# Kernel tuning notes

Measured on AMD Instinct MI355X. Metric: run time of the kernel, lower is better.

The kernel has to match this reference:

```python
import jax, jax.numpy as jnp
import numpy as np

N, E = 50000, 800000
IN_DIM, HIDDEN, OUT_DIM, LAYERS = 128, 64, 40, 3


def setup_inputs() -> dict:
    key = jax.random.key(0)
    ks = jax.random.split(key, 12)
    glorot = lambda k, fi, fo: jax.random.normal(k, (fi, fo), jnp.float32) * np.sqrt(2.0 / (fi + fo)).astype(np.float32)
    return {
        "x": jax.random.normal(ks[0], (N, IN_DIM), jnp.float32),
        "edge_index": jax.random.randint(ks[1], (2, E), 0, N, jnp.int64),
        "edge_weight": jax.random.uniform(ks[2], (E,), jnp.float32),
        "W1": glorot(ks[3], IN_DIM, HIDDEN), "b1": jnp.zeros((HIDDEN,), jnp.float32),
        "W2": glorot(ks[4], HIDDEN, HIDDEN), "b2": jnp.zeros((HIDDEN,), jnp.float32),
        "W3": glorot(ks[5], HIDDEN, HIDDEN), "b3": jnp.zeros((HIDDEN,), jnp.float32),
        "Wlin": glorot(ks[6], HIDDEN * LAYERS, OUT_DIM), "blin": jnp.zeros((OUT_DIM,), jnp.float32),
    }


def reference(x, edge_index, edge_weight, W1, b1, W2, b2, W3, b3, Wlin, blin):
    src, dst = edge_index[0], edge_index[1]

    def gcn_conv(h, W, b):
        # GCNConv with normalize=False: linear transform, then weighted sum aggregation at dst, then bias.
        h = h @ W                                   # [N, hidden]
        msg = h[src] * edge_weight[:, None]          # [E, hidden] gather + scale
        agg = jax.ops.segment_sum(msg, dst, num_segments=h.shape[0])  # scatter-add
        return agg + b

    outs = []
    h = x
    for W, b in ((W1, b1), (W2, b2), (W3, b3)):
        h = jax.nn.relu(gcn_conv(h, W, b))           # dropout is identity at inference
        outs.append(h)

    hjk = jnp.concatenate(outs, axis=-1)             # JumpingKnowledge mode='cat' -> [N, hidden*layers]
    return hjk @ Wlin + blin                         # [N, out_dim]
```

## Files before the change

kernel.cpp:

```cpp
#include <hip/hip_runtime.h>

#define HID 64
#define JK_DIM 192
#define OUT_DIM 40
#define AP 136
#define HP 72

typedef __attribute__((ext_vector_type(8))) short bf16x8;
typedef __attribute__((ext_vector_type(4))) float f32x4;

__device__ inline unsigned short f2b(float f) {
    unsigned u = __float_as_uint(f);
    unsigned r = u + 0x7FFF + ((u >> 16) & 1);
    return (unsigned short)(r >> 16);
}
__device__ inline float b2f(unsigned short u) {
    return __uint_as_float(((unsigned)u) << 16);
}
__device__ inline float blo(unsigned u) { return __uint_as_float(u << 16); }
__device__ inline float bhi(unsigned u) { return __uint_as_float(u & 0xFFFF0000u); }
__device__ inline unsigned pack2(float a, float b) {
    return (unsigned)f2b(a) | ((unsigned)f2b(b) << 16);
}

__global__ __launch_bounds__(256) void hist_gemm(
        const int* __restrict__ dst, int* __restrict__ deg,
        unsigned short* __restrict__ rank, int E, int part,
        int nGemm, int histBlk,
        const float* __restrict__ x, const float* __restrict__ W1,
        unsigned short* __restrict__ linb, int n,
        const float* __restrict__ W2, const float* __restrict__ W3,
        const float* __restrict__ Wlin,
        unsigned short* __restrict__ W2T, unsigned short* __restrict__ W3T,
        unsigned short* __restrict__ WlinT) {
    __shared__ unsigned short Ah[64 * AP];
    __shared__ unsigned short Wt[64 * AP];
    int tid = threadIdx.x;
    int bid = blockIdx.x;
    if (bid >= nGemm + histBlk) {
        int base = (bid - nGemm - histBlk) * 256 + tid;
        int stride = 32 * 256;
        for (int i = base; i < 64 * 64; i += stride) {
            int nn = i >> 6, k = i & 63;
            W2T[i] = f2b(W2[k * 64 + nn]);
            W3T[i] = f2b(W3[k * 64 + nn]);
        }
        for (int i = base; i < 48 * JK_DIM; i += stride) {
            int c = i / JK_DIM, k = i - c * JK_DIM;
            WlinT[i] = (c < OUT_DIM) ? f2b(Wlin[k * OUT_DIM + c]) : (unsigned short)0;
        }
        return;
    }
    if (bid >= nGemm) {
        int hb = bid - nGemm;
        int p = hb & 7;
        int hbid = hb >> 3;
        int nblk = histBlk >> 3;
        int lo = p * part, hi = lo + part;
        int E4 = E >> 2;
        for (int q = hbid * 256 + tid; q < E4; q += nblk * 256) {
            int4 d4 = ((const int4*)dst)[q];
            int e = q * 4;
            if (d4.x >= lo && d4.x < hi) rank[e + 0] = (unsigned short)atomicAdd(&deg[d4.x], 1);
            if (d4.y >= lo && d4.y < hi) rank[e + 1] = (unsigned short)atomicAdd(&deg[d4.y], 1);
            if (d4.z >= lo && d4.z < hi) rank[e + 2] = (unsigned short)atomicAdd(&deg[d4.z], 1);
            if (d4.w >= lo && d4.w < hi) rank[e + 3] = (unsigned short)atomicAdd(&deg[d4.w], 1);
        }
        if (hbid == 0 && tid < (E & 3)) {
            int e = (E & ~3) + tid;
            int d = dst[e];
            if (d >= lo && d < hi) rank[e] = (unsigned short)atomicAdd(&deg[d], 1);
        }
        return;
    }
    int row0 = bid * 64;
    if (row0 >= n) return;
    for (int i = tid; i < 64 * 32; i += 256) {
        int r = i >> 5;
        int c4 = (i & 31) * 4;
        int grow = row0 + r;
        if (grow >= n) grow = n - 1;
        float4 v = *(const float4*)(x + (long)grow * 128 + c4);
        ushort4 o;
        o.x = f2b(v.x); o.y = f2b(v.y); o.z = f2b(v.z); o.w = f2b(v.w);
        *(ushort4*)(Ah + r * AP + c4) = o;
    }
    for (int i = tid; i < 128 * 16; i += 256) {
        int k = i >> 4;
        int n4 = (i & 15) * 4;
        float4 v = *(const float4*)(W1 + (long)k * 64 + n4);
        Wt[(n4 + 0) * AP + k] = f2b(v.x);
        Wt[(n4 + 1) * AP + k] = f2b(v.y);
        Wt[(n4 + 2) * AP + k] = f2b(v.z);
        Wt[(n4 + 3) * AP + k] = f2b(v.w);
    }
    __syncthreads();

    int wave = tid >> 6;
    int lane = tid & 63;
    int lr = lane & 15;
    int lk = (lane >> 4) * 8;
    f32x4 acc[4];
#pragma unroll
    for (int nf = 0; nf < 4; ++nf) acc[nf] = (f32x4){0.f, 0.f, 0.f, 0.f};
#pragma unroll
    for (int k0 = 0; k0 < 128; k0 += 32) {
        bf16x8 a = *(const bf16x8*)(Ah + (wave * 16 + lr) * AP + k0 + lk);
#pragma unroll
        for (int nf = 0; nf < 4; ++nf) {
            bf16x8 b = *(const bf16x8*)(Wt + (nf * 16 + lr) * AP + k0 + lk);
            acc[nf] = __builtin_amdgcn_mfma_f32_16x16x32_bf16(a, b, acc[nf], 0, 0, 0);
        }
    }
    int mbase = wave * 16 + (lane >> 4) * 4;
#pragma unroll
    for (int nf = 0; nf < 4; ++nf) {
#pragma unroll
        for (int r = 0; r < 4; ++r) {
            int grow = row0 + mbase + r;
            if (grow < n)
                linb[(long)grow * HID + nf * 16 + lr] = f2b(acc[nf][r]);
        }
    }
}

__global__ __launch_bounds__(256) void scan_fused(const int* __restrict__ deg,
                                                  int* __restrict__ off,
                                                  int* __restrict__ gctr, int n) {
    __shared__ int tmp[256];
    __shared__ int base;
    int i = blockIdx.x * 256 + threadIdx.x;
    int v = (i < n) ? deg[i] : 0;
    tmp[threadIdx.x] = v;
    __syncthreads();
    for (int d = 1; d < 256; d <<= 1) {
        int t = (threadIdx.x >= d) ? tmp[threadIdx.x - d] : 0;
        __syncthreads();
        tmp[threadIdx.x] += t;
        __syncthreads();
    }
    if (threadIdx.x == 255) base = atomicAdd(gctr, tmp[255]);
    __syncthreads();
    if (i < n) off[i] = base + tmp[threadIdx.x] - v;
}

__global__ __launch_bounds__(256) void fill_csr(
        const int* __restrict__ src, const int* __restrict__ dst,
        const float* __restrict__ ew, const int* __restrict__ off,
        const unsigned short* __restrict__ rank,
        unsigned* __restrict__ ecsr, int E) {
    int tid = threadIdx.x;
    int q = blockIdx.x * 256 + tid;
    int E4 = E >> 2;
    if (q < E4) {
        int4 d4 = ((const int4*)dst)[q];
        int4 s4 = ((const int4*)src)[q];
        float4 wv = ((const float4*)ew)[q];
        ushort4 r4 = ((const ushort4*)rank)[q];
        ecsr[off[d4.x] + r4.x] = (unsigned)s4.x | ((unsigned)f2b(wv.x) << 16);
        ecsr[off[d4.y] + r4.y] = (unsigned)s4.y | ((unsigned)f2b(wv.y) << 16);
        ecsr[off[d4.z] + r4.z] = (unsigned)s4.z | ((unsigned)f2b(wv.z) << 16);
        ecsr[off[d4.w] + r4.w] = (unsigned)s4.w | ((unsigned)f2b(wv.w) << 16);
    }
    if (blockIdx.x == 0 && tid < (E & 3)) {
        int e = (E & ~3) + tid;
        int d = dst[e];
        ecsr[off[d] + rank[e]] = (unsigned)src[e] | ((unsigned)f2b(ew[e]) << 16);
    }
}

__global__ __launch_bounds__(256) void aggregate(const unsigned short* __restrict__ linb,
                                                 const unsigned* __restrict__ ecsr,
                                                 const int* __restrict__ off,
                                                 const int* __restrict__ deg,
                                                 const float* __restrict__ bias,
                                                 unsigned short* __restrict__ hout, int n) {
    int cl = threadIdx.x & 7;
    float4 bLo = *(const float4*)(bias + cl * 8);
    float4 bHi = *(const float4*)(bias + cl * 8 + 4);
    int grp = (blockIdx.x * 256 + threadIdx.x) >> 3;
    int ngrp = (gridDim.x * 256) >> 3;
    for (int node = grp; node < n; node += ngrp) {
        int start = off[node];
        int cnt = deg[node];
        float acc[8];
#pragma unroll
        for (int i = 0; i < 8; ++i) acc[i] = 0.f;

        int s[8];
        float w[8];
#pragma unroll
        for (int t = 0; t < 8; ++t) {
            s[t] = 0; w[t] = 0.f;
            if (t < cnt) {
                unsigned m = ecsr[start + t];
                s[t] = (int)(m & 0xFFFFu);
                w[t] = b2f((unsigned short)(m >> 16));
            }
        }
        for (int bb = 0; bb < cnt; bb += 8) {
            int s2[8];
            float w2[8];
#pragma unroll
            for (int t = 0; t < 8; ++t) {
                int e = bb + 8 + t;
                s2[t] = 0; w2[t] = 0.f;
                if (e < cnt) {
                    unsigned m = ecsr[start + e];
                    s2[t] = (int)(m & 0xFFFFu);
                    w2[t] = b2f((unsigned short)(m >> 16));
                }
            }
            uint4 u[8];
#pragma unroll
            for (int t = 0; t < 8; ++t)
                u[t] = *(const uint4*)(linb + (long)s[t] * HID + cl * 8);
#pragma unroll
            for (int t = 0; t < 8; ++t) {
                acc[0] += blo(u[t].x) * w[t];
                acc[1] += bhi(u[t].x) * w[t];
                acc[2] += blo(u[t].y) * w[t];
                acc[3] += bhi(u[t].y) * w[t];
                acc[4] += blo(u[t].z) * w[t];
                acc[5] += bhi(u[t].z) * w[t];
                acc[6] += blo(u[t].w) * w[t];
                acc[7] += bhi(u[t].w) * w[t];
            }
#pragma unroll
            for (int t = 0; t < 8; ++t) { s[t] = s2[t]; w[t] = w2[t]; }
        }

        uint4 o;
        o.x = pack2(fmaxf(acc[0] + bLo.x, 0.f), fmaxf(acc[1] + bLo.y, 0.f));
        o.y = pack2(fmaxf(acc[2] + bLo.z, 0.f), fmaxf(acc[3] + bLo.w, 0.f));
        o.z = pack2(fmaxf(acc[4] + bHi.x, 0.f), fmaxf(acc[5] + bHi.y, 0.f));
        o.w = pack2(fmaxf(acc[6] + bHi.z, 0.f), fmaxf(acc[7] + bHi.w, 0.f));
        *(uint4*)(hout + (long)node * JK_DIM + cl * 8) = o;
    }
}

__global__ __launch_bounds__(256) void agg_transform(
        const unsigned short* __restrict__ hprev,
        const unsigned* __restrict__ ecsr,
        const int* __restrict__ off, const int* __restrict__ deg,
        const unsigned short* __restrict__ WT, const float* __restrict__ bias,
        unsigned short* __restrict__ hout, int n) {
    __shared__ unsigned short Hs[64 * HP];
    __shared__ unsigned short Wt[64 * HP];
    int tid = threadIdx.x;
    int row0 = blockIdx.x * 64;
    if (row0 >= n) return;
    for (int i = tid; i < 64 * 8; i += 256) {
        int nn = i >> 3;
        int k8 = (i & 7) * 8;
        *(uint4*)(Wt + nn * HP + k8) = *(const uint4*)(WT + nn * 64 + k8);
    }
    int cl = tid & 7;
    int g0 = tid >> 3;
    for (int gi = 0; gi < 2; ++gi) {
        int lrow = g0 + gi * 32;
        int node = row0 + lrow;
        float acc[8];
#pragma unroll
        for (int i = 0; i < 8; ++i) acc[i] = 0.f;
        if (node < n) {
            int start = off[node];
            int cnt = deg[node];
            int s[8];
            float w[8];
#pragma unroll
            for (int t = 0; t < 8; ++t) {
                s[t] = 0; w[t] = 0.f;
                if (t < cnt) {
                    unsigned m = ecsr[start + t];
                    s[t] = (int)(m & 0xFFFFu);
                    w[t] = b2f((unsigned short)(m >> 16));
                }
            }
            for (int bb = 0; bb < cnt; bb += 8) {
                int s2[8];
                float w2[8];
#pragma unroll
                for (int t = 0; t < 8; ++t) {
                    int e = bb + 8 + t;
                    s2[t] = 0; w2[t] = 0.f;
                    if (e < cnt) {
                        unsigned m = ecsr[start + e];
                        s2[t] = (int)(m & 0xFFFFu);
                        w2[t] = b2f((unsigned short)(m >> 16));
                    }
                }
                uint4 u[8];
#pragma unroll
                for (int t = 0; t < 8; ++t)
                    u[t] = *(const uint4*)(hprev + (long)s[t] * JK_DIM + cl * 8);
#pragma unroll
                for (int t = 0; t < 8; ++t) {
                    acc[0] += blo(u[t].x) * w[t];
                    acc[1] += bhi(u[t].x) * w[t];
                    acc[2] += blo(u[t].y) * w[t];
                    acc[3] += bhi(u[t].y) * w[t];
                    acc[4] += blo(u[t].z) * w[t];
                    acc[5] += bhi(u[t].z) * w[t];
                    acc[6] += blo(u[t].w) * w[t];
                    acc[7] += bhi(u[t].w) * w[t];
                }
#pragma unroll
                for (int t = 0; t < 8; ++t) { s[t] = s2[t]; w[t] = w2[t]; }
            }
        }
        uint4 o;
        o.x = pack2(acc[0], acc[1]);
        o.y = pack2(acc[2], acc[3]);
        o.z = pack2(acc[4], acc[5]);
        o.w = pack2(acc[6], acc[7]);
        *(uint4*)(Hs + lrow * HP + cl * 8) = o;
    }
    __syncthreads();
    int wave = tid >> 6;
    int lane = tid & 63;
    int lr = lane & 15;
    int lk = (lane >> 4) * 8;
    f32x4 d[4];
#pragma unroll
    for (int nf = 0; nf < 4; ++nf) d[nf] = (f32x4){0.f, 0.f, 0.f, 0.f};
#pragma unroll
    for (int k0 = 0; k0 < 64; k0 += 32) {
        bf16x8 a = *(const bf16x8*)(Hs + (wave * 16 + lr) * HP + k0 + lk);
#pragma unroll
        for (int nf = 0; nf < 4; ++nf) {
            bf16x8 b = *(const bf16x8*)(Wt + (nf * 16 + lr) * HP + k0 + lk);
            d[nf] = __builtin_amdgcn_mfma_f32_16x16x32_bf16(a, b, d[nf], 0, 0, 0);
        }
    }
    int mbase = wave * 16 + (lane >> 4) * 4;
#pragma unroll
    for (int nf = 0; nf < 4; ++nf) {
        float bv = bias[nf * 16 + lr];
#pragma unroll
        for (int r = 0; r < 4; ++r) {
            int grow = row0 + mbase + r;
            if (grow < n)
                hout[(long)grow * JK_DIM + nf * 16 + lr] = f2b(fmaxf(d[nf][r] + bv, 0.f));
        }
    }
}

__global__ __launch_bounds__(256) void jk_final(
        const unsigned short* __restrict__ hprev,
        const unsigned* __restrict__ ecsr,
        const int* __restrict__ off, const int* __restrict__ deg,
        const unsigned short* __restrict__ W3T, const float* __restrict__ bias,
        const unsigned short* __restrict__ hcat,
        const unsigned short* __restrict__ WlinT,
        const float* __restrict__ blin,
        float* __restrict__ outp, int n) {
    __shared__ unsigned short pool[128 * HP];
    unsigned short* Hs = pool;
    unsigned short* Wt = pool + 64 * HP;
    int tid = threadIdx.x;
    int row0 = blockIdx.x * 64;
    if (row0 >= n) return;
    for (int i = tid; i < 64 * 8; i += 256) {
        int nn = i >> 3;
        int k8 = (i & 7) * 8;
        *(uint4*)(Wt + nn * HP + k8) = *(const uint4*)(W3T + nn * 64 + k8);
    }
    int cl = tid & 7;
    int g0 = tid >> 3;
    for (int gi = 0; gi < 2; ++gi) {
        int lrow = g0 + gi * 32;
        int node = row0 + lrow;
        float acc[8];
#pragma unroll
        for (int i = 0; i < 8; ++i) acc[i] = 0.f;
        if (node < n) {
            int start = off[node];
            int cnt = deg[node];
            int s[8];
            float w[8];
#pragma unroll
            for (int t = 0; t < 8; ++t) {
                s[t] = 0; w[t] = 0.f;
                if (t < cnt) {
                    unsigned m = ecsr[start + t];
                    s[t] = (int)(m & 0xFFFFu);
                    w[t] = b2f((unsigned short)(m >> 16));
                }
            }
            for (int bb = 0; bb < cnt; bb += 8) {
                int s2[8];
                float w2[8];
#pragma unroll
                for (int t = 0; t < 8; ++t) {
                    int e = bb + 8 + t;
                    s2[t] = 0; w2[t] = 0.f;
                    if (e < cnt) {
                        unsigned m = ecsr[start + e];
                        s2[t] = (int)(m & 0xFFFFu);
                        w2[t] = b2f((unsigned short)(m >> 16));
                    }
                }
                uint4 u[8];
#pragma unroll
                for (int t = 0; t < 8; ++t)
                    u[t] = *(const uint4*)(hprev + (long)s[t] * JK_DIM + cl * 8);
#pragma unroll
                for (int t = 0; t < 8; ++t) {
                    acc[0] += blo(u[t].x) * w[t];
                    acc[1] += bhi(u[t].x) * w[t];
                    acc[2] += blo(u[t].y) * w[t];
                    acc[3] += bhi(u[t].y) * w[t];
                    acc[4] += blo(u[t].z) * w[t];
                    acc[5] += bhi(u[t].z) * w[t];
                    acc[6] += blo(u[t].w) * w[t];
                    acc[7] += bhi(u[t].w) * w[t];
                }
#pragma unroll
                for (int t = 0; t < 8; ++t) { s[t] = s2[t]; w[t] = w2[t]; }
            }
        }
        uint4 o;
        o.x = pack2(acc[0], acc[1]);
        o.y = pack2(acc[2], acc[3]);
        o.z = pack2(acc[4], acc[5]);
        o.w = pack2(acc[6], acc[7]);
        *(uint4*)(Hs + lrow * HP + cl * 8) = o;
    }
    __syncthreads();
    int wave = tid >> 6;
    int lane = tid & 63;
    int lr = lane & 15;
    int lk = (lane >> 4) * 8;
    f32x4 d[4];
#pragma unroll
    for (int nf = 0; nf < 4; ++nf) d[nf] = (f32x4){0.f, 0.f, 0.f, 0.f};
#pragma unroll
    for (int k0 = 0; k0 < 64; k0 += 32) {
        bf16x8 a = *(const bf16x8*)(Hs + (wave * 16 + lr) * HP + k0 + lk);
#pragma unroll
        for (int nf = 0; nf < 4; ++nf) {
            bf16x8 b = *(const bf16x8*)(Wt + (nf * 16 + lr) * HP + k0 + lk);
            d[nf] = __builtin_amdgcn_mfma_f32_16x16x32_bf16(a, b, d[nf], 0, 0, 0);
        }
    }
    int mbase = wave * 16 + (lane >> 4) * 4;
    unsigned short* As = Hs;
    unsigned short* WL = Wt;
    f32x4 acc2[3];
#pragma unroll
    for (int nf = 0; nf < 3; ++nf) acc2[nf] = (f32x4){0.f, 0.f, 0.f, 0.f};
    for (int ch = 0; ch < 2; ++ch) {
        int cb = ch * 64;
        __syncthreads();
        for (int i = tid; i < 64 * 8; i += 256) {
            int r = i >> 3;
            int q8 = (i & 7) * 8;
            int grow = row0 + r;
            if (grow >= n) grow = n - 1;
            *(uint4*)(As + r * HP + q8) = *(const uint4*)(hcat + (long)grow * JK_DIM + cb + q8);
        }
        for (int i = tid; i < 48 * 8; i += 256) {
            int c = i >> 3;
            int k8 = (i & 7) * 8;
            *(uint4*)(WL + c * HP + k8) = *(const uint4*)(WlinT + c * JK_DIM + cb + k8);
        }
        __syncthreads();
#pragma unroll
        for (int k0 = 0; k0 < 64; k0 += 32) {
            bf16x8 a = *(const bf16x8*)(As + (wave * 16 + lr) * HP + k0 + lk);
#pragma unroll
            for (int nf = 0; nf < 3; ++nf) {
                bf16x8 b = *(const bf16x8*)(WL + (nf * 16 + lr) * HP + k0 + lk);
                acc2[nf] = __builtin_amdgcn_mfma_f32_16x16x32_bf16(a, b, acc2[nf], 0, 0, 0);
            }
        }
    }
    __syncthreads();
#pragma unroll
    for (int nf = 0; nf < 4; ++nf) {
        float bv = bias[nf * 16 + lr];
#pragma unroll
        for (int r = 0; r < 4; ++r)
            As[(mbase + r) * HP + nf * 16 + lr] = f2b(fmaxf(d[nf][r] + bv, 0.f));
    }
    for (int i = tid; i < 48 * 8; i += 256) {
        int c = i >> 3;
        int k8 = (i & 7) * 8;
        *(uint4*)(WL + c * HP + k8) = *(const uint4*)(WlinT + c * JK_DIM + 128 + k8);
    }
    __syncthreads();
#pragma unroll
    for (int k0 = 0; k0 < 64; k0 += 32) {
        bf16x8 a = *(const bf16x8*)(As + (wave * 16 + lr) * HP + k0 + lk);
#pragma unroll
        for (int nf = 0; nf < 3; ++nf) {
            bf16x8 b = *(const bf16x8*)(WL + (nf * 16 + lr) * HP + k0 + lk);
            acc2[nf] = __builtin_amdgcn_mfma_f32_16x16x32_bf16(a, b, acc2[nf], 0, 0, 0);
        }
    }
#pragma unroll
    for (int nf = 0; nf < 3; ++nf) {
        int col = nf * 16 + lr;
        if (col < OUT_DIM) {
            float bb = blin[col];
#pragma unroll
            for (int r = 0; r < 4; ++r) {
                int grow = row0 + mbase + r;
                if (grow < n)
                    outp[(long)grow * OUT_DIM + col] = acc2[nf][r] + bb;
            }
        }
    }
}

extern "C" void kernel_launch(void* const* d_in, const int* in_sizes, int n_in,
                              void* d_out, int out_size, void* d_ws, size_t ws_size,
                              hipStream_t stream) {
    const float* x    = (const float*)d_in[0];
    const int*   ei   = (const int*)d_in[1];
    const float* ew   = (const float*)d_in[2];
    const float* W1   = (const float*)d_in[3];
    const float* b1   = (const float*)d_in[4];
    const float* W2   = (const float*)d_in[5];
    const float* b2   = (const float*)d_in[6];
    const float* W3   = (const float*)d_in[7];
    const float* b3   = (const float*)d_in[8];
    const float* Wlin = (const float*)d_in[9];
    const float* blin = (const float*)d_in[10];
    float* out = (float*)d_out;

    const int N = in_sizes[0] / 128;
    const int E = in_sizes[2];
    const int* src = ei;
    const int* dst = ei + E;
    const int PART = (N + 7) / 8;

    char* wsb = (char*)d_ws;
    unsigned short* linb  = (unsigned short*)wsb;   wsb += (long)N * HID * 2;
    unsigned short* hcatb = (unsigned short*)wsb;   wsb += (long)N * JK_DIM * 2;
    char* zbase = wsb;
    int* deg    = (int*)wsb;                        wsb += (long)N * 4;
    int* off    = (int*)wsb;                        wsb += (long)N * 4;
    int* bsum   = (int*)wsb;                        wsb += 256 * 4;
    size_t zbytes = (size_t)(wsb - zbase);
    unsigned short* W2T  = (unsigned short*)wsb;    wsb += 64 * 64 * 2;
    unsigned short* W3T  = (unsigned short*)wsb;    wsb += 64 * 64 * 2;
    unsigned short* WlinT = (unsigned short*)wsb;   wsb += 48 * JK_DIM * 2;
    unsigned* ecsr = (unsigned*)wsb;
    unsigned short* rank = hcatb;
    int* gctr = bsum;

    dim3 blk(256);
    const int nblkN = (N + 255) / 256;
    dim3 gN(nblkN);
    const int nGemm = (N + 63) / 64;
    const int histBlk = 8 * 104;
    dim3 gHG(nGemm + histBlk + 32);
    const int nFill = ((E >> 2) + 255) / 256;
    dim3 gFill(nFill);
    dim3 gTile((N + 63) / 64);
    dim3 gAgg((N + 31) / 32);

    unsigned short* h1 = hcatb;
    unsigned short* h2 = hcatb + HID;

    hipMemsetAsync(zbase, 0, zbytes, stream);

    hist_gemm<<<gHG, blk, 0, stream>>>(dst, deg, rank, E, PART, nGemm, histBlk,
                                       x, W1, linb, N, W2, W3, Wlin,
                                       W2T, W3T, WlinT);
    scan_fused<<<gN, blk, 0, stream>>>(deg, off, gctr, N);
    fill_csr<<<gFill, blk, 0, stream>>>(src, dst, ew, off, rank, ecsr, E);

    aggregate<<<gAgg, blk, 0, stream>>>(linb, ecsr, off, deg, b1, h1, N);
    agg_transform<<<gTile, blk, 0, stream>>>(h1, ecsr, off, deg, W2T, b2, h2, N);
    jk_final<<<gTile, blk, 0, stream>>>(h2, ecsr, off, deg, W3T, b3,
                                        hcatb, WlinT, blin, out, N);
}
```

Baseline: 228.5 us.

## Fuse all GCN stages into one persistent kernel with software grid barriers

Replaces the six separate kernel launches (histogram+GEMM, scan, CSR fill, three aggregation layers) with a single persistent 'mega' kernel. The grid is sized from the occupancy query and the stages are separated by an atomic-counter grid barrier. The intent is to remove launch gaps and the memset of the degree array, which is now zeroed inside the kernel. In exchange, grid-stride loops replace one-block-per-tile mapping, and barrier spinning costs extra. Correctness depends on all blocks being co-resident, and the grid size assumes 256 CUs.

```diff
diff --git a/kernel.cpp b/kernel.cpp
--- a/kernel.cpp
+++ b/kernel.cpp
@@ -23,136 +23,155 @@
     return (unsigned)f2b(a) | ((unsigned)f2b(b) << 16);
 }
 
-__global__ __launch_bounds__(256) void hist_gemm(
-        const int* __restrict__ dst, int* __restrict__ deg,
-        unsigned short* __restrict__ rank, int E, int part,
-        int nGemm, int histBlk,
-        const float* __restrict__ x, const float* __restrict__ W1,
-        unsigned short* __restrict__ linb, int n,
-        const float* __restrict__ W2, const float* __restrict__ W3,
-        const float* __restrict__ Wlin,
+__device__ inline void gbar(int* cnt, int* gen, int nb) {
+    __syncthreads();
+    if (threadIdx.x == 0) {
+        int g = __hip_atomic_load(gen, __ATOMIC_RELAXED, __HIP_MEMORY_SCOPE_AGENT);
+        int v = __hip_atomic_fetch_add(cnt, 1, __ATOMIC_ACQ_REL, __HIP_MEMORY_SCOPE_AGENT);
+        if (v == nb - 1) {
+            __hip_atomic_store(cnt, 0, __ATOMIC_RELAXED, __HIP_MEMORY_SCOPE_AGENT);
+            __hip_atomic_store(gen, g + 1, __ATOMIC_RELEASE, __HIP_MEMORY_SCOPE_AGENT);
+        } else {
+            while (__hip_atomic_load(gen, __ATOMIC_ACQUIRE, __HIP_MEMORY_SCOPE_AGENT) == g)
+                __builtin_amdgcn_s_sleep(4);
+        }
+    }
+    __syncthreads();
+}
+
+__global__ __launch_bounds__(256) void mega(
+        const int* __restrict__ src, const int* __restrict__ dst,
+        const float* __restrict__ ew, const float* __restrict__ x,
+        const float* __restrict__ W1, const float* __restrict__ b1,
+        const float* __restrict__ W2, const float* __restrict__ b2,
+        const float* __restrict__ W3, const float* __restrict__ b3,
+        const float* __restrict__ Wlin, const float* __restrict__ blin,
+        float* __restrict__ out,
+        int* __restrict__ deg, int* __restrict__ off, int* __restrict__ gctr,
+        int* __restrict__ bcnt, int* __restrict__ bgen,
+        unsigned short* __restrict__ rank, unsigned* __restrict__ ecsr,
+        unsigned short* __restrict__ linb, unsigned short* __restrict__ hcatb,
         unsigned short* __restrict__ W2T, unsigned short* __restrict__ W3T,
-        unsigned short* __restrict__ WlinT) {
-    __shared__ unsigned short Ah[64 * AP];
-    __shared__ unsigned short Wt[64 * AP];
+        unsigned short* __restrict__ WlinT,
+        int N, int E, int part, int histBlk, int nblkN, int nTiles) {
+    __shared__ unsigned short lds[64 * AP * 2];
     int tid = threadIdx.x;
     int bid = blockIdx.x;
-    if (bid >= nGemm + histBlk) {
-        int base = (bid - nGemm - histBlk) * 256 + tid;
-        int stride = 32 * 256;
-        for (int i = base; i < 64 * 64; i += stride) {
+    int nb = gridDim.x;
+    int E4 = E >> 2;
+    unsigned short* h1 = hcatb;
+    unsigned short* h2 = hcatb + HID;
+
+    for (int i = bid * 256 + tid; i < N; i += nb * 256) deg[i] = 0;
+    gbar(bcnt, bgen, nb);
+
+    {
+        unsigned short* Ah = lds;
+        unsigned short* Wt = lds + 64 * AP;
+        for (int t = bid; t < nTiles; t += nb) {
+            int row0 = t * 64;
+            __syncthreads();
+            for (int i = tid; i < 64 * 32; i += 256) {
+                int r = i >> 5;
+                int c4 = (i & 31) * 4;
+                int grow = row0 + r;
+                if (grow >= N) grow = N - 1;
+                float4 v = *(const float4*)(x + (long)grow * 128 + c4);
+                ushort4 o;
+                o.x = f2b(v.x); o.y = f2b(v.y); o.z = f2b(v.z); o.w = f2b(v.w);
+                *(ushort4*)(Ah + r * AP + c4) = o;
+            }
+            for (int i = tid; i < 128 * 16; i += 256) {
+                int k = i >> 4;
+                int n4 = (i & 15) * 4;
+                float4 v = *(const float4*)(W1 + (long)k * 64 + n4);
+                Wt[(n4 + 0) * AP + k] = f2b(v.x);
+                Wt[(n4 + 1) * AP + k] = f2b(v.y);
+                Wt[(n4 + 2) * AP + k] = f2b(v.z);
+                Wt[(n4 + 3) * AP + k] = f2b(v.w);
+            }
+            __syncthreads();
+            int wave = tid >> 6;
+            int lane = tid & 63;
+            int lr = lane & 15;
+            int lk = (lane >> 4) * 8;
+            f32x4 acc[4];
+#pragma unroll
+            for (int nf = 0; nf < 4; ++nf) acc[nf] = (f32x4){0.f, 0.f, 0.f, 0.f};
+#pragma unroll
+            for (int k0 = 0; k0 < 128; k0 += 32) {
+                bf16x8 a = *(const bf16x8*)(Ah + (wave * 16 + lr) * AP + k0 + lk);
+#pragma unroll
+                for (int nf = 0; nf < 4; ++nf) {
+                    bf16x8 b = *(const bf16x8*)(Wt + (nf * 16 + lr) * AP + k0 + lk);
+                    acc[nf] = __builtin_amdgcn_mfma_f32_16x16x32_bf16(a, b, acc[nf], 0, 0, 0);
+                }
+            }
+            int mbase = wave * 16 + (lane >> 4) * 4;
+#pragma unroll
+            for (int nf = 0; nf < 4; ++nf) {
+#pragma unroll
+                for (int r = 0; r < 4; ++r) {
+                    int grow = row0 + mbase + r;
+                    if (grow < N)
+                        linb[(long)grow * HID + nf * 16 + lr] = f2b(acc[nf][r]);
+                }
+            }
+        }
+        int nblk = histBlk >> 3;
+        for (int h = bid; h < histBlk; h += nb) {
+            int p = h & 7;
+            int hbid = h >> 3;
+            int lo = p * part, hi = lo + part;
+            for (int q = hbid * 256 + tid; q < E4; q += nblk * 256) {
+                int4 d4 = ((const int4*)dst)[q];
+                int e = q * 4;
+                if (d4.x >= lo && d4.x < hi) rank[e + 0] = (unsigned short)atomicAdd(&deg[d4.x], 1);
+                if (d4.y >= lo && d4.y < hi) rank[e + 1] = (unsigned short)atomicAdd(&deg[d4.y], 1);
+                if (d4.z >= lo && d4.z < hi) rank[e + 2] = (unsigned short)atomicAdd(&deg[d4.z], 1);
+                if (d4.w >= lo && d4.w < hi) rank[e + 3] = (unsigned short)atomicAdd(&deg[d4.w], 1);
+            }
+            if (h < 8 && tid < (E & 3)) {
+                int e = (E & ~3) + tid;
+                int d = dst[e];
+                if (d >= lo && d < hi) rank[e] = (unsigned short)atomicAdd(&deg[d], 1);
+            }
+        }
+        for (int i = bid * 256 + tid; i < 64 * 64; i += nb * 256) {
             int nn = i >> 6, k = i & 63;
             W2T[i] = f2b(W2[k * 64 + nn]);
             W3T[i] = f2b(W3[k * 64 + nn]);
         }
-        for (int i = base; i < 48 * JK_DIM; i += stride) {
+        for (int i = bid * 256 + tid; i < 48 * JK_DIM; i += nb * 256) {
             int c = i / JK_DIM, k = i - c * JK_DIM;
             WlinT[i] = (c < OUT_DIM) ? f2b(Wlin[k * OUT_DIM + c]) : (unsigned short)0;
         }
-        return;
-    }
-    if (bid >= nGemm) {
-        int hb = bid - nGemm;
-        int p = hb & 7;
-        int hbid = hb >> 3;
-        int nblk = histBlk >> 3;
-        int lo = p * part, hi = lo + part;
-        int E4 = E >> 2;
-        for (int q = hbid * 256 + tid; q < E4; q += nblk * 256) {
-            int4 d4 = ((const int4*)dst)[q];
-            int e = q * 4;
-            if (d4.x >= lo && d4.x < hi) rank[e + 0] = (unsigned short)atomicAdd(&deg[d4.x], 1);
-            if (d4.y >= lo && d4.y < hi) rank[e + 1] = (unsigned short)atomicAdd(&deg[d4.y], 1);
-            if (d4.z >= lo && d4.z < hi) rank[e + 2] = (unsigned short)atomicAdd(&deg[d4.z], 1);
-            if (d4.w >= lo && d4.w < hi) rank[e + 3] = (unsigned short)atomicAdd(&deg[d4.w], 1);
-        }
-        if (hbid == 0 && tid < (E & 3)) {
-            int e = (E & ~3) + tid;
-            int d = dst[e];
-            if (d >= lo && d < hi) rank[e] = (unsigned short)atomicAdd(&deg[d], 1);
-        }
-        return;
-    }
-    int row0 = bid * 64;
-    if (row0 >= n) return;
-    for (int i = tid; i < 64 * 32; i += 256) {
-        int r = i >> 5;
-        int c4 = (i & 31) * 4;
-        int grow = row0 + r;
-        if (grow >= n) grow = n - 1;
-        float4 v = *(const float4*)(x + (long)grow * 128 + c4);
-        ushort4 o;
-        o.x = f2b(v.x); o.y = f2b(v.y); o.z = f2b(v.z); o.w = f2b(v.w);
-        *(ushort4*)(Ah + r * AP + c4) = o;
-    }
-    for (int i = tid; i < 128 * 16; i += 256) {
-        int k = i >> 4;
-        int n4 = (i & 15) * 4;
-        float4 v = *(const float4*)(W1 + (long)k * 64 + n4);
-        Wt[(n4 + 0) * AP + k] = f2b(v.x);
-        Wt[(n4 + 1) * AP + k] = f2b(v.y);
-        Wt[(n4 + 2) * AP + k] = f2b(v.z);
-        Wt[(n4 + 3) * AP + k] = f2b(v.w);
-    }
-    __syncthreads();
-
-    int wave = tid >> 6;
-    int lane = tid & 63;
-    int lr = lane & 15;
-    int lk = (lane >> 4) * 8;
-    f32x4 acc[4];
-#pragma unroll
-    for (int nf = 0; nf < 4; ++nf) acc[nf] = (f32x4){0.f, 0.f, 0.f, 0.f};
-#pragma unroll
-    for (int k0 = 0; k0 < 128; k0 += 32) {
-        bf16x8 a = *(const bf16x8*)(Ah + (wave * 16 + lr) * AP + k0 + lk);
-#pragma unroll
-        for (int nf = 0; nf < 4; ++nf) {
-            bf16x8 b = *(const bf16x8*)(Wt + (nf * 16 + lr) * AP + k0 + lk);
-            acc[nf] = __builtin_amdgcn_mfma_f32_16x16x32_bf16(a, b, acc[nf], 0, 0, 0);
-        }
-    }
-    int mbase = wave * 16 + (lane >> 4) * 4;
-#pragma unroll
-    for (int nf = 0; nf < 4; ++nf) {
-#pragma unroll
-        for (int r = 0; r < 4; ++r) {
-            int grow = row0 + mbase + r;
-            if (grow < n)
-                linb[(long)grow * HID + nf * 16 + lr] = f2b(acc[nf][r]);
-        }
-    }
-}
-
-__global__ __launch_bounds__(256) void scan_fused(const int* __restrict__ deg,
-                                                  int* __restrict__ off,
-                                                  int* __restrict__ gctr, int n) {
-    __shared__ int tmp[256];
-    __shared__ int base;
-    int i = blockIdx.x * 256 + threadIdx.x;
-    int v = (i < n) ? deg[i] : 0;
-    tmp[threadIdx.x] = v;
-    __syncthreads();
-    for (int d = 1; d < 256; d <<= 1) {
-        int t = (threadIdx.x >= d) ? tmp[threadIdx.x - d] : 0;
-        __syncthreads();
-        tmp[threadIdx.x] += t;
-        __syncthreads();
-    }
-    if (threadIdx.x == 255) base = atomicAdd(gctr, tmp[255]);
-    __syncthreads();
-    if (i < n) off[i] = base + tmp[threadIdx.x] - v;
-}
-
-__global__ __launch_bounds__(256) void fill_csr(
-        const int* __restrict__ src, const int* __restrict__ dst,
-        const float* __restrict__ ew, const int* __restrict__ off,
-        const unsigned short* __restrict__ rank,
-        unsigned* __restrict__ ecsr, int E) {
-    int tid = threadIdx.x;
-    int q = blockIdx.x * 256 + tid;
-    int E4 = E >> 2;
-    if (q < E4) {
+    }
+    gbar(bcnt, bgen, nb);
+
+    {
+        int* tmp = (int*)lds;
+        int* basep = (int*)lds + 256;
+        for (int c = bid; c < nblkN; c += nb) {
+            int i = c * 256 + tid;
+            int v = (i < N) ? deg[i] : 0;
+            __syncthreads();
+            tmp[tid] = v;
+            __syncthreads();
+            for (int d = 1; d < 256; d <<= 1) {
+                int t = (tid >= d) ? tmp[tid - d] : 0;
+                __syncthreads();
+                tmp[tid] += t;
+                __syncthreads();
+            }
+            if (tid == 255) basep[0] = atomicAdd(gctr, tmp[255]);
+            __syncthreads();
+            if (i < N) off[i] = basep[0] + tmp[tid] - v;
+        }
+    }
+    gbar(bcnt, bgen, nb);
+
+    for (int q = bid * 256 + tid; q < E4; q += nb * 256) {
         int4 d4 = ((const int4*)dst)[q];
         int4 s4 = ((const int4*)src)[q];
         float4 wv = ((const float4*)ew)[q];
@@ -162,110 +181,25 @@
         ecsr[off[d4.z] + r4.z] = (unsigned)s4.z | ((unsigned)f2b(wv.z) << 16);
         ecsr[off[d4.w] + r4.w] = (unsigned)s4.w | ((unsigned)f2b(wv.w) << 16);
     }
-    if (blockIdx.x == 0 && tid < (E & 3)) {
+    if (bid == 0 && tid < (E & 3)) {
         int e = (E & ~3) + tid;
         int d = dst[e];
         ecsr[off[d] + rank[e]] = (unsigned)src[e] | ((unsigned)f2b(ew[e]) << 16);
     }
-}
-
-__global__ __launch_bounds__(256) void aggregate(const unsigned short* __restrict__ linb,
-                                                 const unsigned* __restrict__ ecsr,
-                                                 const int* __restrict__ off,
-                                                 const int* __restrict__ deg,
-                                                 const float* __restrict__ bias,
-                                                 unsigned short* __restrict__ hout, int n) {
-    int cl = threadIdx.x & 7;
-    float4 bLo = *(const float4*)(bias + cl * 8);
-    float4 bHi = *(const float4*)(bias + cl * 8 + 4);
-    int grp = (blockIdx.x * 256 + threadIdx.x) >> 3;
-    int ngrp = (gridDim.x * 256) >> 3;
-    for (int node = grp; node < n; node += ngrp) {
-        int start = off[node];
-        int cnt = deg[node];
-        float acc[8];
-#pragma unroll
-        for (int i = 0; i < 8; ++i) acc[i] = 0.f;
-
-        int s[8];
-        float w[8];
-#pragma unroll
-        for (int t = 0; t < 8; ++t) {
-            s[t] = 0; w[t] = 0.f;
-            if (t < cnt) {
-                unsigned m = ecsr[start + t];
-                s[t] = (int)(m & 0xFFFFu);
-                w[t] = b2f((unsigned short)(m >> 16));
-            }
-        }
-        for (int bb = 0; bb < cnt; bb += 8) {
-            int s2[8];
-            float w2[8];
-#pragma unroll
-            for (int t = 0; t < 8; ++t) {
-                int e = bb + 8 + t;
-                s2[t] = 0; w2[t] = 0.f;
-                if (e < cnt) {
-                    unsigned m = ecsr[start + e];
-                    s2[t] = (int)(m & 0xFFFFu);
-                    w2[t] = b2f((unsigned short)(m >> 16));
-                }
-            }
-            uint4 u[8];
-#pragma unroll
-            for (int t = 0; t < 8; ++t)
-                u[t] = *(const uint4*)(linb + (long)s[t] * HID + cl * 8);
-#pragma unroll
-            for (int t = 0; t < 8; ++t) {
-                acc[0] += blo(u[t].x) * w[t];
-                acc[1] += bhi(u[t].x) * w[t];
-                acc[2] += blo(u[t].y) * w[t];
-                acc[3] += bhi(u[t].y) * w[t];
-                acc[4] += blo(u[t].z) * w[t];
-                acc[5] += bhi(u[t].z) * w[t];
-                acc[6] += blo(u[t].w) * w[t];
-                acc[7] += bhi(u[t].w) * w[t];
-            }
-#pragma unroll
-            for (int t = 0; t < 8; ++t) { s[t] = s2[t]; w[t] = w2[t]; }
-        }
-
-        uint4 o;
-        o.x = pack2(fmaxf(acc[0] + bLo.x, 0.f), fmaxf(acc[1] + bLo.y, 0.f));
-        o.y = pack2(fmaxf(acc[2] + bLo.z, 0.f), fmaxf(acc[3] + bLo.w, 0.f));
-        o.z = pack2(fmaxf(acc[4] + bHi.x, 0.f), fmaxf(acc[5] + bHi.y, 0.f));
-        o.w = pack2(fmaxf(acc[6] + bHi.z, 0.f), fmaxf(acc[7] + bHi.w, 0.f));
-        *(uint4*)(hout + (long)node * JK_DIM + cl * 8) = o;
-    }
-}
-
-__global__ __launch_bounds__(256) void agg_transform(
-        const unsigned short* __restrict__ hprev,
-        const unsigned* __restrict__ ecsr,
-        const int* __restrict__ off, const int* __restrict__ deg,
-        const unsigned short* __restrict__ WT, const float* __restrict__ bias,
-        unsigned short* __restrict__ hout, int n) {
-    __shared__ unsigned short Hs[64 * HP];
-    __shared__ unsigned short Wt[64 * HP];
-    int tid = threadIdx.x;
-    int row0 = blockIdx.x * 64;
-    if (row0 >= n) return;
-    for (int i = tid; i < 64 * 8; i += 256) {
-        int nn = i >> 3;
-        int k8 = (i & 7) * 8;
-        *(uint4*)(Wt + nn * HP + k8) = *(const uint4*)(WT + nn * 64 + k8);
-    }
-    int cl = tid & 7;
-    int g0 = tid >> 3;
-    for (int gi = 0; gi < 2; ++gi) {
-        int lrow = g0 + gi * 32;
-        int node = row0 + lrow;
-        float acc[8];
-#pragma unroll
-        for (int i = 0; i < 8; ++i) acc[i] = 0.f;
-        if (node < n) {
+    gbar(bcnt, bgen, nb);
+
+    {
+        int cl = tid & 7;
+        float4 bLo = *(const float4*)(b1 + cl * 8);
+        float4 bHi = *(const float4*)(b1 + cl * 8 + 4);
+        int grp = (bid * 256 + tid) >> 3;
+        int ngrp = (nb * 256) >> 3;
+        for (int node = grp; node < N; node += ngrp) {
             int start = off[node];
             int cnt = deg[node];
+            float acc[8];
+#pragma unroll
+            for (int i = 0; i < 8; ++i) acc[i] = 0.f;
             int s[8];
             float w[8];
 #pragma unroll
@@ -293,7 +227,7 @@
                 uint4 u[8];
 #pragma unroll
                 for (int t = 0; t < 8; ++t)
-                    u[t] = *(const uint4*)(hprev + (long)s[t] * JK_DIM + cl * 8);
+                    u[t] = *(const uint4*)(linb + (long)s[t] * HID + cl * 8);
 #pragma unroll
                 for (int t = 0; t < 8; ++t) {
                     acc[0] += blo(u[t].x) * w[t];
@@ -308,208 +242,279 @@
 #pragma unroll
                 for (int t = 0; t < 8; ++t) { s[t] = s2[t]; w[t] = w2[t]; }
             }
-        }
-        uint4 o;
-        o.x = pack2(acc[0], acc[1]);
-        o.y = pack2(acc[2], acc[3]);
-        o.z = pack2(acc[4], acc[5]);
-        o.w = pack2(acc[6], acc[7]);
-        *(uint4*)(Hs + lrow * HP + cl * 8) = o;
-    }
-    __syncthreads();
-    int wave = tid >> 6;
-    int lane = tid & 63;
-    int lr = lane & 15;
-    int lk = (lane >> 4) * 8;
-    f32x4 d[4];
-#pragma unroll
-    for (int nf = 0; nf < 4; ++nf) d[nf] = (f32x4){0.f, 0.f, 0.f, 0.f};
-#pragma unroll
-    for (int k0 = 0; k0 < 64; k0 += 32) {
-        bf16x8 a = *(const bf16x8*)(Hs + (wave * 16 + lr) * HP + k0 + lk);
-#pragma unroll
-        for (int nf = 0; nf < 4; ++nf) {
-            bf16x8 b = *(const bf16x8*)(Wt + (nf * 16 + lr) * HP + k0 + lk);
-            d[nf] = __builtin_amdgcn_mfma_f32_16x16x32_bf16(a, b, d[nf], 0, 0, 0);
-        }
-    }
-    int mbase = wave * 16 + (lane >> 4) * 4;
-#pragma unroll
-    for (int nf = 0; nf < 4; ++nf) {
-        float bv = bias[nf * 16 + lr];
-#pragma unroll
-        for (int r = 0; r < 4; ++r) {
-            int grow = row0 + mbase + r;
-            if (grow < n)
-                hout[(long)grow * JK_DIM + nf * 16 + lr] = f2b(fmaxf(d[nf][r] + bv, 0.f));
-        }
-    }
-}
-
-__global__ __launch_bounds__(256) void jk_final(
-        const unsigned short* __restrict__ hprev,
-        const unsigned* __restrict__ ecsr,
-        const int* __restrict__ off, const int* __restrict__ deg,
-        const unsigned short* __restrict__ W3T, const float* __restrict__ bias,
-        const unsigned short* __restrict__ hcat,
-        const unsigned short* __restrict__ WlinT,
-        const float* __restrict__ blin,
-        float* __restrict__ outp, int n) {
-    __shared__ unsigned short pool[128 * HP];
-    unsigned short* Hs = pool;
-    unsigned short* Wt = pool + 64 * HP;
-    int tid = threadIdx.x;
-    int row0 = blockIdx.x * 64;
-    if (row0 >= n) return;
-    for (int i = tid; i < 64 * 8; i += 256) {
-        int nn = i >> 3;
-        int k8 = (i & 7) * 8;
-        *(uint4*)(Wt + nn * HP + k8) = *(const uint4*)(W3T + nn * 64 + k8);
-    }
-    int cl = tid & 7;
-    int g0 = tid >> 3;
-    for (int gi = 0; gi < 2; ++gi) {
-        int lrow = g0 + gi * 32;
-        int node = row0 + lrow;
-        float acc[8];
-#pragma unroll
-        for (int i = 0; i < 8; ++i) acc[i] = 0.f;
-        if (node < n) {
-            int start = off[node];
-            int cnt = deg[node];
-            int s[8];
-            float w[8];
-#pragma unroll
-            for (int t = 0; t < 8; ++t) {
-                s[t] = 0; w[t] = 0.f;
-                if (t < cnt) {
-                    unsigned m = ecsr[start + t];
-                    s[t] = (int)(m & 0xFFFFu);
-                    w[t] = b2f((unsigned short)(m >> 16));
-                }
-            }
-            for (int bb = 0; bb < cnt; bb += 8) {
-                int s2[8];
-                float w2[8];
-#pragma unroll
-                for (int t = 0; t < 8; ++t) {
-                    int e = bb + 8 + t;
-                    s2[t] = 0; w2[t] = 0.f;
-                    if (e < cnt) {
-                        unsigned m = ecsr[start + e];
-                        s2[t] = (int)(m & 0xFFFFu);
-                        w2[t] = b2f((unsigned short)(m >> 16));
-                    }
-                }
-                uint4 u[8];
-#pragma unroll
-                for (int t = 0; t < 8; ++t)
-                    u[t] = *(const uint4*)(hprev + (long)s[t] * JK_DIM + cl * 8);
-#pragma unroll
-                for (int t = 0; t < 8; ++t) {
-                    acc[0] += blo(u[t].x) * w[t];
-                    acc[1] += bhi(u[t].x) * w[t];
-                    acc[2] += blo(u[t].y) * w[t];
-                    acc[3] += bhi(u[t].y) * w[t];
-                    acc[4] += blo(u[t].z) * w[t];
-                    acc[5] += bhi(u[t].z) * w[t];
-                    acc[6] += blo(u[t].w) * w[t];
-                    acc[7] += bhi(u[t].w) * w[t];
-                }
-#pragma unroll
-                for (int t = 0; t < 8; ++t) { s[t] = s2[t]; w[t] = w2[t]; }
-            }
-        }
-        uint4 o;
-        o.x = pack2(acc[0], acc[1]);
-        o.y = pack2(acc[2], acc[3]);
-        o.z = pack2(acc[4], acc[5]);
-        o.w = pack2(acc[6], acc[7]);
-        *(uint4*)(Hs + lrow * HP + cl * 8) = o;
-    }
-    __syncthreads();
-    int wave = tid >> 6;
-    int lane = tid & 63;
-    int lr = lane & 15;
-    int lk = (lane >> 4) * 8;
-    f32x4 d[4];
-#pragma unroll
-    for (int nf = 0; nf < 4; ++nf) d[nf] = (f32x4){0.f, 0.f, 0.f, 0.f};
-#pragma unroll
-    for (int k0 = 0; k0 < 64; k0 += 32) {
-        bf16x8 a = *(const bf16x8*)(Hs + (wave * 16 + lr) * HP + k0 + lk);
-#pragma unroll
-        for (int nf = 0; nf < 4; ++nf) {
-            bf16x8 b = *(const bf16x8*)(Wt + (nf * 16 + lr) * HP + k0 + lk);
-            d[nf] = __builtin_amdgcn_mfma_f32_16x16x32_bf16(a, b, d[nf], 0, 0, 0);
-        }
-    }
-    int mbase = wave * 16 + (lane >> 4) * 4;
-    unsigned short* As = Hs;
-    unsigned short* WL = Wt;
-    f32x4 acc2[3];
-#pragma unroll
-    for (int nf = 0; nf < 3; ++nf) acc2[nf] = (f32x4){0.f, 0.f, 0.f, 0.f};
-    for (int ch = 0; ch < 2; ++ch) {
-        int cb = ch * 64;
-        __syncthreads();
-        for (int i = tid; i < 64 * 8; i += 256) {
-            int r = i >> 3;
-            int q8 = (i & 7) * 8;
-            int grow = row0 + r;
-            if (grow >= n) grow = n - 1;
-            *(uint4*)(As + r * HP + q8) = *(const uint4*)(hcat + (long)grow * JK_DIM + cb + q8);
-        }
-        for (int i = tid; i < 48 * 8; i += 256) {
-            int c = i >> 3;
-            int k8 = (i & 7) * 8;
-            *(uint4*)(WL + c * HP + k8) = *(const uint4*)(WlinT + c * JK_DIM + cb + k8);
-        }
-        __syncthreads();
-#pragma unroll
-        for (int k0 = 0; k0 < 64; k0 += 32) {
-            bf16x8 a = *(const bf16x8*)(As + (wave * 16 + lr) * HP + k0 + lk);
+            uint4 o;
+            o.x = pack2(fmaxf(acc[0] + bLo.x, 0.f), fmaxf(acc[1] + bLo.y, 0.f));
+            o.y = pack2(fmaxf(acc[2] + bLo.z, 0.f), fmaxf(acc[3] + bLo.w, 0.f));
+            o.z = pack2(fmaxf(acc[4] + bHi.x, 0.f), fmaxf(acc[5] + bHi.y, 0.f));
+            o.w = pack2(fmaxf(acc[6] + bHi.z, 0.f), fmaxf(acc[7] + bHi.w, 0.f));
+            *(uint4*)(h1 + (long)node * JK_DIM + cl * 8) = o;
+        }
+    }
+    gbar(bcnt, bgen, nb);
+
+    {
+        unsigned short* Hs = lds;
+        unsigned short* Wt = lds + 64 * HP;
+        for (int t = bid; t < nTiles; t += nb) {
+            int row0 = t * 64;
+            __syncthreads();
+            for (int i = tid; i < 64 * 8; i += 256) {
+                int nn = i >> 3;
+                int k8 = (i & 7) * 8;
+                *(uint4*)(Wt + nn * HP + k8) = *(const uint4*)(W2T + nn * 64 + k8);
+            }
+            int cl = tid & 7;
+            int g0 = tid >> 3;
+            for (int gi = 0; gi < 2; ++gi) {
+                int lrow = g0 + gi * 32;
+                int node = row0 + lrow;
+                float acc[8];
+#pragma unroll
+                for (int i = 0; i < 8; ++i) acc[i] = 0.f;
+                if (node < N) {
+                    int start = off[node];
+                    int cnt = deg[node];
+                    int s[8];
+                    float w[8];
+#pragma unroll
+                    for (int t2 = 0; t2 < 8; ++t2) {
+                        s[t2] = 0; w[t2] = 0.f;
+                        if (t2 < cnt) {
+                            unsigned m = ecsr[start + t2];
+                            s[t2] = (int)(m & 0xFFFFu);
+                            w[t2] = b2f((unsigned short)(m >> 16));
+                        }
+                    }
+                    for (int bb = 0; bb < cnt; bb += 8) {
+                        int s2[8];
+                        float w2[8];
+#pragma unroll
+                        for (int t2 = 0; t2 < 8; ++t2) {
+                            int e = bb + 8 + t2;
+                            s2[t2] = 0; w2[t2] = 0.f;
+                            if (e < cnt) {
+                                unsigned m = ecsr[start + e];
+                                s2[t2] = (int)(m & 0xFFFFu);
+                                w2[t2] = b2f((unsigned short)(m >> 16));
+                            }
+                        }
+                        uint4 u[8];
+#pragma unroll
+                        for (int t2 = 0; t2 < 8; ++t2)
+                            u[t2] = *(const uint4*)(h1 + (long)s[t2] * JK_DIM + cl * 8);
+#pragma unroll
+                        for (int t2 = 0; t2 < 8; ++t2) {
+                            acc[0] += blo(u[t2].x) * w[t2];
+                            acc[1] += bhi(u[t2].x) * w[t2];
+                            acc[2] += blo(u[t2].y) * w[t2];
+                            acc[3] += bhi(u[t2].y) * w[t2];
+                            acc[4] += blo(u[t2].z) * w[t2];
+                            acc[5] += bhi(u[t2].z) * w[t2];
+                            acc[6] += blo(u[t2].w) * w[t2];
+                            acc[7] += bhi(u[t2].w) * w[t2];
+                        }
+#pragma unroll
+                        for (int t2 = 0; t2 < 8; ++t2) { s[t2] = s2[t2]; w[t2] = w2[t2]; }
+                    }
+                }
+                uint4 o;
+                o.x = pack2(acc[0], acc[1]);
+                o.y = pack2(acc[2], acc[3]);
+                o.z = pack2(acc[4], acc[5]);
+                o.w = pack2(acc[6], acc[7]);
+                *(uint4*)(Hs + lrow * HP + cl * 8) = o;
+            }
+            __syncthreads();
+            int wave = tid >> 6;
+            int lane = tid & 63;
+            int lr = lane & 15;
+            int lk = (lane >> 4) * 8;
+            f32x4 d[4];
+#pragma unroll
+            for (int nf = 0; nf < 4; ++nf) d[nf] = (f32x4){0.f, 0.f, 0.f, 0.f};
+#pragma unroll
+            for (int k0 = 0; k0 < 64; k0 += 32) {
+                bf16x8 a = *(const bf16x8*)(Hs + (wave * 16 + lr) * HP + k0 + lk);
+#pragma unroll
+                for (int nf = 0; nf < 4; ++nf) {
+                    bf16x8 b = *(const bf16x8*)(Wt + (nf * 16 + lr) * HP + k0 + lk);
+                    d[nf] = __builtin_amdgcn_mfma_f32_16x16x32_bf16(a, b, d[nf], 0, 0, 0);
+                }
+            }
+            int mbase = wave * 16 + (lane >> 4) * 4;
+#pragma unroll
+            for (int nf = 0; nf < 4; ++nf) {
+                float bv = b2[nf * 16 + lr];
+#pragma unroll
+                for (int r = 0; r < 4; ++r) {
+                    int grow = row0 + mbase + r;
+                    if (grow < N)
+                        h2[(long)grow * JK_DIM + nf * 16 + lr] = f2b(fmaxf(d[nf][r] + bv, 0.f));
+                }
+            }
+            __syncthreads();
+        }
+    }
+    gbar(bcnt, bgen, nb);
+
+    {
+        unsigned short* Hs = lds;
+        unsigned short* Wt = lds + 64 * HP;
+        for (int t = bid; t < nTiles; t += nb) {
+            int row0 = t * 64;
+            __syncthreads();
+            for (int i = tid; i < 64 * 8; i += 256) {
+                int nn = i >> 3;
+                int k8 = (i & 7) * 8;
+                *(uint4*)(Wt + nn * HP + k8) = *(const uint4*)(W3T + nn * 64 + k8);
+            }
+            int cl = tid & 7;
+            int g0 = tid >> 3;
+            for (int gi = 0; gi < 2; ++gi) {
+                int lrow = g0 + gi * 32;
+                int node = row0 + lrow;
+                float acc[8];
+#pragma unroll
+                for (int i = 0; i < 8; ++i) acc[i] = 0.f;
+                if (node < N) {
+                    int start = off[node];
+                    int cnt = deg[node];
+                    int s[8];
+                    float w[8];
+#pragma unroll
+                    for (int t2 = 0; t2 < 8; ++t2) {
+                        s[t2] = 0; w[t2] = 0.f;
+                        if (t2 < cnt) {
+                            unsigned m = ecsr[start + t2];
+                            s[t2] = (int)(m & 0xFFFFu);
+                            w[t2] = b2f((unsigned short)(m >> 16));
+                        }
+                    }
+                    for (int bb = 0; bb < cnt; bb += 8) {
+                        int s2[8];
+                        float w2[8];
+#pragma unroll
+                        for (int t2 = 0; t2 < 8; ++t2) {
+                            int e = bb + 8 + t2;
+                            s2[t2] = 0; w2[t2] = 0.f;
+                            if (e < cnt) {
+                                unsigned m = ecsr[start + e];
+                                s2[t2] = (int)(m & 0xFFFFu);
+                                w2[t2] = b2f((unsigned short)(m >> 16));
+                            }
+                        }
+                        uint4 u[8];
+#pragma unroll
+                        for (int t2 = 0; t2 < 8; ++t2)
+                            u[t2] = *(const uint4*)(h2 + (long)s[t2] * JK_DIM + cl * 8);
+#pragma unroll
+                        for (int t2 = 0; t2 < 8; ++t2) {
+                            acc[0] += blo(u[t2].x) * w[t2];
+                            acc[1] += bhi(u[t2].x) * w[t2];
+                            acc[2] += blo(u[t2].y) * w[t2];
+                            acc[3] += bhi(u[t2].y) * w[t2];
+                            acc[4] += blo(u[t2].z) * w[t2];
+                            acc[5] += bhi(u[t2].z) * w[t2];
+                            acc[6] += blo(u[t2].w) * w[t2];
+                            acc[7] += bhi(u[t2].w) * w[t2];
+                        }
+#pragma unroll
+                        for (int t2 = 0; t2 < 8; ++t2) { s[t2] = s2[t2]; w[t2] = w2[t2]; }
+                    }
+                }
+                uint4 o;
+                o.x = pack2(acc[0], acc[1]);
+                o.y = pack2(acc[2], acc[3]);
+                o.z = pack2(acc[4], acc[5]);
+                o.w = pack2(acc[6], acc[7]);
+                *(uint4*)(Hs + lrow * HP + cl * 8) = o;
+            }
+            __syncthreads();
+            int wave = tid >> 6;
+            int lane = tid & 63;
+            int lr = lane & 15;
+            int lk = (lane >> 4) * 8;
+            f32x4 d[4];
+#pragma unroll
+            for (int nf = 0; nf < 4; ++nf) d[nf] = (f32x4){0.f, 0.f, 0.f, 0.f};
+#pragma unroll
+            for (int k0 = 0; k0 < 64; k0 += 32) {
+                bf16x8 a = *(const bf16x8*)(Hs + (wave * 16 + lr) * HP + k0 + lk);
+#pragma unroll
+                for (int nf = 0; nf < 4; ++nf) {
+                    bf16x8 b = *(const bf16x8*)(Wt + (nf * 16 + lr) * HP + k0 + lk);
+                    d[nf] = __builtin_amdgcn_mfma_f32_16x16x32_bf16(a, b, d[nf], 0, 0, 0);
+                }
+            }
+            int mbase = wave * 16 + (lane >> 4) * 4;
+            unsigned short* As = Hs;
+            unsigned short* WL = Wt;
+            f32x4 acc2[3];
+#pragma unroll
+            for (int nf = 0; nf < 3; ++nf) acc2[nf] = (f32x4){0.f, 0.f, 0.f, 0.f};
+            for (int ch = 0; ch < 2; ++ch) {
+                int cb = ch * 64;
+                __syncthreads();
+                for (int i = tid; i < 64 * 8; i += 256) {
+                    int r = i >> 3;
+                    int q8 = (i & 7) * 8;
+                    int grow = row0 + r;
+                    if (grow >= N) grow = N - 1;
+                    *(uint4*)(As + r * HP + q8) = *(const uint4*)(hcatb + (long)grow * JK_DIM + cb + q8);
+                }
+                for (int i = tid; i < 48 * 8; i += 256) {
+                    int c = i >> 3;
+                    int k8 = (i & 7) * 8;
+                    *(uint4*)(WL + c * HP + k8) = *(const uint4*)(WlinT + c * JK_DIM + cb + k8);
+                }
+                __syncthreads();
+#pragma unroll
+                for (int k0 = 0; k0 < 64; k0 += 32) {
+                    bf16x8 a = *(const bf16x8*)(As + (wave * 16 + lr) * HP + k0 + lk);
+#pragma unroll
+                    for (int nf = 0; nf < 3; ++nf) {
+                        bf16x8 b = *(const bf16x8*)(WL + (nf * 16 + lr) * HP + k0 + lk);
+                        acc2[nf] = __builtin_amdgcn_mfma_f32_16x16x32_bf16(a, b, acc2[nf], 0, 0, 0);
+                    }
+                }
+            }
+            __syncthreads();
+#pragma unroll
+            for (int nf = 0; nf < 4; ++nf) {
+                float bv = b3[nf * 16 + lr];
+#pragma unroll
+                for (int r = 0; r < 4; ++r)
+                    As[(mbase + r) * HP + nf * 16 + lr] = f2b(fmaxf(d[nf][r] + bv, 0.f));
+            }
+            for (int i = tid; i < 48 * 8; i += 256) {
+                int c = i >> 3;
+                int k8 = (i & 7) * 8;
+                *(uint4*)(WL + c * HP + k8) = *(const uint4*)(WlinT + c * JK_DIM + 128 + k8);
+            }
+            __syncthreads();
+#pragma unroll
+            for (int k0 = 0; k0 < 64; k0 += 32) {
+                bf16x8 a = *(const bf16x8*)(As + (wave * 16 + lr) * HP + k0 + lk);
+#pragma unroll
+                for (int nf = 0; nf < 3; ++nf) {
+                    bf16x8 b = *(const bf16x8*)(WL + (nf * 16 + lr) * HP + k0 + lk);
+                    acc2[nf] = __builtin_amdgcn_mfma_f32_16x16x32_bf16(a, b, acc2[nf], 0, 0, 0);
+                }
+            }
 #pragma unroll
             for (int nf = 0; nf < 3; ++nf) {
-                bf16x8 b = *(const bf16x8*)(WL + (nf * 16 + lr) * HP + k0 + lk);
-                acc2[nf] = __builtin_amdgcn_mfma_f32_16x16x32_bf16(a, b, acc2[nf], 0, 0, 0);
-            }
-        }
-    }
-    __syncthreads();
-#pragma unroll
-    for (int nf = 0; nf < 4; ++nf) {
-        float bv = bias[nf * 16 + lr];
-#pragma unroll
-        for (int r = 0; r < 4; ++r)
-            As[(mbase + r) * HP + nf * 16 + lr] = f2b(fmaxf(d[nf][r] + bv, 0.f));
-    }
-    for (int i = tid; i < 48 * 8; i += 256) {
-        int c = i >> 3;
-        int k8 = (i & 7) * 8;
-        *(uint4*)(WL + c * HP + k8) = *(const uint4*)(WlinT + c * JK_DIM + 128 + k8);
-    }
-    __syncthreads();
-#pragma unroll
-    for (int k0 = 0; k0 < 64; k0 += 32) {
-        bf16x8 a = *(const bf16x8*)(As + (wave * 16 + lr) * HP + k0 + lk);
-#pragma unroll
-        for (int nf = 0; nf < 3; ++nf) {
-            bf16x8 b = *(const bf16x8*)(WL + (nf * 16 + lr) * HP + k0 + lk);
-            acc2[nf] = __builtin_amdgcn_mfma_f32_16x16x32_bf16(a, b, acc2[nf], 0, 0, 0);
-        }
-    }
-#pragma unroll
-    for (int nf = 0; nf < 3; ++nf) {
-        int col = nf * 16 + lr;
-        if (col < OUT_DIM) {
-            float bb = blin[col];
-#pragma unroll
-            for (int r = 0; r < 4; ++r) {
-                int grow = row0 + mbase + r;
-                if (grow < n)
-                    outp[(long)grow * OUT_DIM + col] = acc2[nf][r] + bb;
-            }
+                int col = nf * 16 + lr;
+                if (col < OUT_DIM) {
+                    float bb = blin[col];
+#pragma unroll
+                    for (int r = 0; r < 4; ++r) {
+                        int grow = row0 + mbase + r;
+                        if (grow < N)
+                            out[(long)grow * OUT_DIM + col] = acc2[nf][r] + bb;
+                    }
+                }
+            }
+            __syncthreads();
         }
     }
 }
@@ -530,51 +535,44 @@
     const float* blin = (const float*)d_in[10];
     float* out = (float*)d_out;
 
-    const int N = in_sizes[0] / 128;
-    const int E = in_sizes[2];
+    int N = in_sizes[0] / 128;
+    int E = in_sizes[2];
     const int* src = ei;
     const int* dst = ei + E;
-    const int PART = (N + 7) / 8;
+    int PART = (N + 7) / 8;
 
     char* wsb = (char*)d_ws;
     unsigned short* linb  = (unsigned short*)wsb;   wsb += (long)N * HID * 2;
     unsigned short* hcatb = (unsigned short*)wsb;   wsb += (long)N * JK_DIM * 2;
-    char* zbase = wsb;
     int* deg    = (int*)wsb;                        wsb += (long)N * 4;
     int* off    = (int*)wsb;                        wsb += (long)N * 4;
     int* bsum   = (int*)wsb;                        wsb += 256 * 4;
-    size_t zbytes = (size_t)(wsb - zbase);
     unsigned short* W2T  = (unsigned short*)wsb;    wsb += 64 * 64 * 2;
     unsigned short* W3T  = (unsigned short*)wsb;    wsb += 64 * 64 * 2;
     unsigned short* WlinT = (unsigned short*)wsb;   wsb += 48 * JK_DIM * 2;
     unsigned* ecsr = (unsigned*)wsb;
     unsigned short* rank = hcatb;
     int* gctr = bsum;
-
-    dim3 blk(256);
-    const int nblkN = (N + 255) / 256;
-    dim3 gN(nblkN);
-    const int nGemm = (N + 63) / 64;
-    const int histBlk = 8 * 104;
-    dim3 gHG(nGemm + histBlk + 32);
-    const int nFill = ((E >> 2) + 255) / 256;
-    dim3 gFill(nFill);
-    dim3 gTile((N + 63) / 64);
-    dim3 gAgg((N + 31) / 32);
-
-    unsigned short* h1 = hcatb;
-    unsigned short* h2 = hcatb + HID;
-
-    hipMemsetAsync(zbase, 0, zbytes, stream);
-
-    hist_gemm<<<gHG, blk, 0, stream>>>(dst, deg, rank, E, PART, nGemm, histBlk,
-                                       x, W1, linb, N, W2, W3, Wlin,
-                                       W2T, W3T, WlinT);
-    scan_fused<<<gN, blk, 0, stream>>>(deg, off, gctr, N);
-    fill_csr<<<gFill, blk, 0, stream>>>(src, dst, ew, off, rank, ecsr, E);
-
-    aggregate<<<gAgg, blk, 0, stream>>>(linb, ecsr, off, deg, b1, h1, N);
-    agg_transform<<<gTile, blk, 0, stream>>>(h1, ecsr, off, deg, W2T, b2, h2, N);
-    jk_final<<<gTile, blk, 0, stream>>>(h2, ecsr, off, deg, W3T, b3,
-                                        hcatb, WlinT, blin, out, N);
+    int* bcnt = bsum + 1;
+    int* bgen = bsum + 2;
+
+    int nTiles = (N + 63) / 64;
+    int histBlk = 8 * 104;
+    int nblkN = (N + 255) / 256;
+
+    static int s_cap = 0;
+    if (s_cap == 0) {
+        int mb = 0;
+        if (hipOccupancyMaxActiveBlocksPerMultiprocessor(&mb, mega, 256, 0) != hipSuccess || mb < 1)
+            mb = 2;
+        s_cap = mb * 256;
+    }
+    int nb = nTiles < s_cap ? nTiles : s_cap;
+
+    hipMemsetAsync(bsum, 0, 4 * sizeof(int), stream);
+
+    mega<<<dim3(nb), dim3(256), 0, stream>>>(
+        src, dst, ew, x, W1, b1, W2, b2, W3, b3, Wlin, blin, out,
+        deg, off, gctr, bcnt, bgen, rank, ecsr, linb, hcatb,
+        W2T, W3T, WlinT, N, E, PART, histBlk, nblkN, nTiles);
 }
```

New measurement: 631.9 us. 2.77x slower.
